# Kernel optimization log

Hardware: AMD Instinct MI355X
Metric: run time of the kernel (lower is better)

## Reference

```python
import jax, jax.numpy as jnp
import numpy as np

N, E, G = 40000, 640000, 64
D_IN, D_EMB, D_HID, D_OUT = 128, 128, 128, 36


def setup_inputs() -> dict:
    key = jax.random.key(0)
    ks = jax.random.split(key, 12)
    x = jax.random.normal(ks[0], (N, D_IN), dtype=jnp.float32)
    edge_weight = jax.random.uniform(ks[1], (E,), dtype=jnp.float32)
    rho = jax.random.uniform(ks[2], (G,), dtype=jnp.float32)
    edge_index = jax.random.randint(ks[3], (2, E), 0, N, dtype=jnp.int32)
    batch = jnp.sort(jax.random.randint(ks[4], (N,), 0, G, dtype=jnp.int32))
    def lin(k, fi, fo):
        s = 1.0 / np.sqrt(fi)
        return jax.random.normal(k, (fi, fo), dtype=jnp.float32) * s
    conv_w = lin(ks[5], D_IN, D_EMB)
    conv_b = jnp.zeros((D_EMB,), jnp.float32)
    w1 = lin(ks[6], 2 * D_EMB + 1, D_HID); b1 = jnp.zeros((D_HID,), jnp.float32)
    w2 = lin(ks[7], D_HID, D_HID);        b2 = jnp.zeros((D_HID,), jnp.float32)
    w3 = lin(ks[8], D_HID, D_OUT);        b3 = jnp.zeros((D_OUT,), jnp.float32)
    return dict(x=x, edge_weight=edge_weight, rho=rho, conv_w=conv_w, conv_b=conv_b,
                w1=w1, b1=b1, w2=w2, b2=b2, w3=w3, b3=b3,
                edge_index=edge_index, batch=batch)


def _gcn_conv(h, edge_index, ew, W, b):
    # PyG GCNConv: add self-loops (weight 1), symmetric deg^-1/2 normalization,
    # linear transform, gather-scale-scatter aggregation, bias.
    n = h.shape[0]
    loop = jnp.arange(n, dtype=edge_index.dtype)
    src = jnp.concatenate([edge_index[0], loop])
    dst = jnp.concatenate([edge_index[1], loop])
    w_all = jnp.concatenate([ew, jnp.ones((n,), ew.dtype)])
    deg = jax.ops.segment_sum(w_all, dst, num_segments=n)
    dinv = jnp.where(deg > 0, jax.lax.rsqrt(deg), 0.0)
    norm = dinv[src] * w_all * dinv[dst]          # [E+N]
    hW = h @ W                                    # [N, D_EMB]
    msg = hW[src] * norm[:, None]                 # [E+N, D_EMB]
    return jax.ops.segment_sum(msg, dst, num_segments=n) + b


def reference(x, edge_weight, rho, conv_w, conv_b, w1, b1, w2, b2, w3, b3,
              edge_index, batch):
    h = jax.nn.relu(_gcn_conv(x, edge_index, edge_weight, conv_w, conv_b))
    g = G
    cnt = jax.ops.segment_sum(jnp.ones((h.shape[0],), h.dtype), batch, num_segments=g)
    hmax = jax.ops.segment_max(h, batch, num_segments=g)
    hmax = jnp.where(cnt[:, None] > 0, hmax, 0.0)
    hsum = jax.ops.segment_sum(h, batch, num_segments=g)
    hmean = hsum / jnp.maximum(cnt, 1.0)[:, None]
    hg = jnp.concatenate([hmax, hmean, rho[:, None]], axis=1)  # [G, 2*D_EMB+1]
    z = jax.nn.relu(hg @ w1 + b1)
    z = jax.nn.relu(z @ w2 + b2)
    return z @ w3 + b3
```

## Files before the change

### kernel.cpp

```cpp
#include <hip/hip_runtime.h>
#include <hip/hip_fp16.h>

static __device__ __forceinline__ float relu_f(float v) { return v > 0.f ? v : 0.f; }

typedef _Float16 half8 __attribute__((ext_vector_type(8)));
typedef float floatx4 __attribute__((ext_vector_type(4)));

#define ELL 96

static __device__ __forceinline__ float entry_w(unsigned int pk) {
  return __half2float(__ushort_as_half((unsigned short)(pk >> 16)));
}


__global__ void init_kernel(unsigned long long* __restrict__ cnt, int n,
                            float* __restrict__ gmax, float* __restrict__ gsum,
                            float* __restrict__ gcnt, int gch, int g,
                            const float* __restrict__ W, _Float16* __restrict__ wt) {
  int i = blockIdx.x * blockDim.x + threadIdx.x;
  if (i < n) cnt[i] = 0ull;
  if (i < gch) { gmax[i] = 0.f; gsum[i] = 0.f; }
  if (i < g) gcnt[i] = 0.f;
  if (i < 128 * 128) {
    int k = i >> 7, nn = i & 127;
    wt[nn * 128 + k] = (_Float16)W[i];
  }
}


__global__ void count_fill_kernel(const int* __restrict__ src, const int* __restrict__ dst,
                                  const float* __restrict__ ew,
                                  unsigned long long* __restrict__ cnt,
                                  unsigned int* __restrict__ epack, int E) {
  int e = blockIdx.x * blockDim.x + threadIdx.x;
  if (e >= E) return;
  int d = dst[e];
  float w = ew[e];
  unsigned long long pk = (1ull << 32) | (unsigned long long)__float2uint_rn(w * 16777216.f);
  unsigned long long old = atomicAdd(&cnt[d], pk);
  unsigned int r = (unsigned int)(old >> 32);
  if (r < ELL) {
    unsigned short w16 = __half_as_ushort(__float2half_rn(w));
    epack[(size_t)d * ELL + r] = (unsigned int)src[e] | ((unsigned int)w16 << 16);
  }
}


__global__ void premul_cast_kernel(const float4* __restrict__ x4,
                                   const unsigned long long* __restrict__ cnt,
                                   half8* __restrict__ xh8, int n) {
  int j = blockIdx.x * blockDim.x + threadIdx.x;
  if (j >= n * 16) return;
  int node = j >> 4;
  unsigned long long cv = cnt[node];
  float deg = 1.f + (float)(unsigned int)cv * (1.f / 16777216.f);
  float dinv = rsqrtf(deg);
  float4 a = x4[2 * j], b = x4[2 * j + 1];
  half8 o;
  o[0] = (_Float16)(a.x * dinv); o[1] = (_Float16)(a.y * dinv);
  o[2] = (_Float16)(a.z * dinv); o[3] = (_Float16)(a.w * dinv);
  o[4] = (_Float16)(b.x * dinv); o[5] = (_Float16)(b.y * dinv);
  o[6] = (_Float16)(b.z * dinv); o[7] = (_Float16)(b.w * dinv);
  xh8[j] = o;
}


__global__ __launch_bounds__(256) void agg_gemm_pool_kernel(const half8* __restrict__ xh8,
    const unsigned long long* __restrict__ cnt,
    const unsigned int* __restrict__ epack, const _Float16* __restrict__ wt,
    const float* __restrict__ bias, const int* __restrict__ batch,
    float* __restrict__ gmax, float* __restrict__ gsum, float* __restrict__ gcnt, int n) {
  __shared__ float sH[64 * 129];
  _Float16* sAgg = (_Float16*)sH;
  __shared__ int sBatch[64];
  int tid = threadIdx.x;
  int w = tid >> 6, lane = tid & 63;
  int grp = lane >> 4, sub = lane & 15;
  int quad = lane >> 4, c15 = lane & 15;
  int row0 = blockIdx.x * 64;
  int nb = n - row0; if (nb > 64) nb = 64;

  #pragma unroll
  for (int it = 0; it < 4; ++it) {
    int rloc = w * 16 + it * 4 + grp;
    int node = row0 + rloc;
    if (node >= n) node = n - 1;
    unsigned long long cv = cnt[node];
    int deg = (int)(unsigned int)(cv >> 32);
    if (deg > ELL) deg = ELL;
    float dn = rsqrtf(1.f + (float)(unsigned int)cv * (1.f / 16777216.f));
    half8 xv = xh8[(size_t)node * 16 + sub];
    float acc[8];
    #pragma unroll
    for (int c = 0; c < 8; ++c) acc[c] = dn * (float)xv[c];
    size_t base = (size_t)node * ELL;
    int dlen = (deg + 7) & ~7;
    for (int j = 0; j < dlen; j += 8) {
      uint4 pa = *(const uint4*)&epack[base + j];
      uint4 pb = *(const uint4*)&epack[base + j + 4];
      unsigned int pk[8] = {pa.x, pa.y, pa.z, pa.w, pb.x, pb.y, pb.z, pb.w};
      half8 hx[8];
      #pragma unroll
      for (int u = 0; u < 8; ++u) {
        int sidx = (j + u < deg) ? (int)(pk[u] & 0xFFFFu) : node;
        hx[u] = xh8[(size_t)sidx * 16 + sub];
      }
      #pragma unroll
      for (int u = 0; u < 8; ++u) {
        float wgt = (j + u < deg) ? entry_w(pk[u]) * dn : 0.f;
        #pragma unroll
        for (int c = 0; c < 8; ++c) acc[c] += wgt * (float)hx[u][c];
      }
    }
    half8 outv;
    #pragma unroll
    for (int c = 0; c < 8; ++c) outv[c] = (_Float16)acc[c];
    *(half8*)&sAgg[rloc * 136 + sub * 8] = outv;
  }
  __syncthreads();

  half8 af[4];
  #pragma unroll
  for (int ks = 0; ks < 4; ++ks)
    af[ks] = *(const half8*)&sAgg[(w * 16 + c15) * 136 + ks * 32 + quad * 8];
  if (tid < nb) sBatch[tid] = batch[row0 + tid];
  __syncthreads();

  float bb[8];
  #pragma unroll
  for (int j = 0; j < 8; ++j) bb[j] = bias[j * 16 + c15];

  floatx4 acc[8] = {};
  #pragma unroll
  for (int ks = 0; ks < 4; ++ks) {
    #pragma unroll
    for (int j = 0; j < 8; ++j) {
      const half8* bptr =
          (const half8*)(wt + (size_t)(j * 16 + c15) * 128 + ks * 32 + quad * 8);
      acc[j] = __builtin_amdgcn_mfma_f32_16x16x32_f16(af[ks], *bptr, acc[j], 0, 0, 0);
    }
  }

  #pragma unroll
  for (int j = 0; j < 8; ++j) {
    int col = j * 16 + c15;
    #pragma unroll
    for (int r = 0; r < 4; ++r) {
      int row = w * 16 + quad * 4 + r;
      if (row < nb) sH[row * 129 + col] = relu_f(acc[j][r] + bb[j]);
    }
  }
  __syncthreads();

  if (tid < 128) {
    int c = tid;
    int cur = sBatch[0];
    float mx = 0.f, sm = 0.f;
    int cnt_ = 0;
    for (int r = 0; r < nb; ++r) {
      int g = sBatch[r];
      if (g != cur) {
        atomicMax((int*)&gmax[cur * 128 + c], __float_as_int(mx));
        atomicAdd(&gsum[cur * 128 + c], sm);
        if (c == 0) atomicAdd(&gcnt[cur], (float)cnt_);
        mx = 0.f; sm = 0.f; cnt_ = 0; cur = g;
      }
      float v = sH[r * 129 + c];
      mx = fmaxf(mx, v);
      sm += v;
      ++cnt_;
    }
    atomicMax((int*)&gmax[cur * 128 + c], __float_as_int(mx));
    atomicAdd(&gsum[cur * 128 + c], sm);
    if (c == 0) atomicAdd(&gcnt[cur], (float)cnt_);
  }
}


__global__ __launch_bounds__(128) void mlp_kernel(const float* __restrict__ gmax,
    const float* __restrict__ gsum, const float* __restrict__ gcnt,
    const float* __restrict__ rho,
    const float* __restrict__ w1, const float* __restrict__ b1,
    const float* __restrict__ w2, const float* __restrict__ b2,
    const float* __restrict__ w3, const float* __restrict__ b3,
    float* __restrict__ out) {
  __shared__ float s_in[257];
  __shared__ float s_z1[128];
  __shared__ float s_z2[128];
  int g = blockIdx.x, t = threadIdx.x;
  float inv_cnt = 1.f / fmaxf(gcnt[g], 1.f);
  s_in[t] = gmax[g * 128 + t];
  s_in[128 + t] = gsum[g * 128 + t] * inv_cnt;
  if (t == 0) s_in[256] = rho[g];
  __syncthreads();
  float s = b1[t];
  for (int k = 0; k < 257; ++k) s += s_in[k] * w1[k * 128 + t];
  s_z1[t] = relu_f(s);
  __syncthreads();
  s = b2[t];
  for (int k = 0; k < 128; ++k) s += s_z1[k] * w2[k * 128 + t];
  s_z2[t] = relu_f(s);
  __syncthreads();
  if (t < 36) {
    s = b3[t];
    for (int k = 0; k < 128; ++k) s += s_z2[k] * w3[k * 36 + t];
    out[g * 36 + t] = s;
  }
}


extern "C" void kernel_launch(void* const* d_in, const int* in_sizes, int n_in,
                              void* d_out, int out_size, void* d_ws, size_t ws_size,
                              hipStream_t stream) {
  const float* x      = (const float*)d_in[0];
  const float* ew     = (const float*)d_in[1];
  const float* rho    = (const float*)d_in[2];
  const float* conv_w = (const float*)d_in[3];
  const float* conv_b = (const float*)d_in[4];
  const float* w1 = (const float*)d_in[5];
  const float* b1 = (const float*)d_in[6];
  const float* w2 = (const float*)d_in[7];
  const float* b2 = (const float*)d_in[8];
  const float* w3 = (const float*)d_in[9];
  const float* b3 = (const float*)d_in[10];
  const int* eidx  = (const int*)d_in[11];
  const int* batch = (const int*)d_in[12];

  const int N = in_sizes[0] / 128;
  const int E = in_sizes[1];
  const int G = in_sizes[2];
  const int* srcp = eidx;
  const int* dstp = eidx + E;

  char* p = (char*)d_ws;
  auto carve = [&](size_t bytes) { char* r = p; p += (bytes + 255) & ~(size_t)255; return (void*)r; };
  unsigned long long* cnt  = (unsigned long long*)carve((size_t)N * 8);
  unsigned int*       epack = (unsigned int*)     carve((size_t)N * ELL * 4);
  half8*              xh    = (half8*)            carve((size_t)N * 128 * 2);
  _Float16*           wt    = (_Float16*)         carve((size_t)128 * 128 * 2);
  float*              gmax  = (float*)            carve((size_t)G * 128 * 4);
  float*              gsum  = (float*)            carve((size_t)G * 128 * 4);
  float*              gcnt  = (float*)            carve((size_t)G * 4);

  int m = N;
  if (G * 128 > m) m = G * 128;
  if (128 * 128 > m) m = 128 * 128;

  init_kernel<<<(m + 255) / 256, 256, 0, stream>>>(cnt, N, gmax, gsum, gcnt,
                                                   G * 128, G, conv_w, wt);
  count_fill_kernel<<<(E + 255) / 256, 256, 0, stream>>>(srcp, dstp, ew, cnt, epack, E);
  premul_cast_kernel<<<(N * 16 + 255) / 256, 256, 0, stream>>>((const float4*)x, cnt, xh, N);
  agg_gemm_pool_kernel<<<(N + 63) / 64, 256, 0, stream>>>(xh, cnt, epack, wt, conv_b,
                                                          batch, gmax, gsum, gcnt, N);
  mlp_kernel<<<G, 128, 0, stream>>>(gmax, gsum, gcnt, rho, w1, b1, w2, b2, w3, b3,
                                    (float*)d_out);
}
```

Baseline: 190.9 us.

## Replace init kernel with memset, vectorize edge fill, prefetch ELL rows, split MLP

Removes the separate init kernel by grouping the zeroed buffers contiguously and clearing them with one hipMemsetAsync, and folds the weight transpose into the edge-fill kernel. The fill kernel now loads four edges per thread with vector loads. The aggregation loop software-prefetches the next ELL chunk of packed edges. The MLP runs with 256 threads, splitting each dot product across two halves and reducing through shared memory. Together these aim to cut launch count, memory-load latency and serial MLP depth, at the cost of extra registers and shared-memory syncs.

New measurement: 210.2 us. +10.1%, slower.

```diff
diff --git a/kernel.cpp b/kernel.cpp
--- a/kernel.cpp
+++ b/kernel.cpp
@@ -13,35 +13,48 @@
 }
 
 
-__global__ void init_kernel(unsigned long long* __restrict__ cnt, int n,
-                            float* __restrict__ gmax, float* __restrict__ gsum,
-                            float* __restrict__ gcnt, int gch, int g,
-                            const float* __restrict__ W, _Float16* __restrict__ wt) {
+__global__ __launch_bounds__(256) void count_fill_kernel(
+    const int* __restrict__ src, const int* __restrict__ dst,
+    const float* __restrict__ ew, unsigned long long* __restrict__ cnt,
+    unsigned int* __restrict__ epack, int E,
+    const float* __restrict__ W, _Float16* __restrict__ wt) {
   int i = blockIdx.x * blockDim.x + threadIdx.x;
-  if (i < n) cnt[i] = 0ull;
-  if (i < gch) { gmax[i] = 0.f; gsum[i] = 0.f; }
-  if (i < g) gcnt[i] = 0.f;
   if (i < 128 * 128) {
     int k = i >> 7, nn = i & 127;
     wt[nn * 128 + k] = (_Float16)W[i];
   }
-}
-
-
-__global__ void count_fill_kernel(const int* __restrict__ src, const int* __restrict__ dst,
-                                  const float* __restrict__ ew,
-                                  unsigned long long* __restrict__ cnt,
-                                  unsigned int* __restrict__ epack, int E) {
-  int e = blockIdx.x * blockDim.x + threadIdx.x;
-  if (e >= E) return;
-  int d = dst[e];
-  float w = ew[e];
-  unsigned long long pk = (1ull << 32) | (unsigned long long)__float2uint_rn(w * 16777216.f);
-  unsigned long long old = atomicAdd(&cnt[d], pk);
-  unsigned int r = (unsigned int)(old >> 32);
-  if (r < ELL) {
-    unsigned short w16 = __half_as_ushort(__float2half_rn(w));
-    epack[(size_t)d * ELL + r] = (unsigned int)src[e] | ((unsigned int)w16 << 16);
+  int e0 = i * 4;
+  if (e0 >= E) return;
+  if (e0 + 3 < E) {
+    int4   s4 = *(const int4*)(src + e0);
+    int4   d4 = *(const int4*)(dst + e0);
+    float4 w4 = *(const float4*)(ew + e0);
+    int   ss[4] = {s4.x, s4.y, s4.z, s4.w};
+    int   dd[4] = {d4.x, d4.y, d4.z, d4.w};
+    float ww[4] = {w4.x, w4.y, w4.z, w4.w};
+    #pragma unroll
+    for (int u = 0; u < 4; ++u) {
+      unsigned long long pk = (1ull << 32) |
+          (unsigned long long)__float2uint_rn(ww[u] * 16777216.f);
+      unsigned long long old = atomicAdd(&cnt[dd[u]], pk);
+      unsigned int r = (unsigned int)(old >> 32);
+      if (r < ELL) {
+        unsigned short w16 = __half_as_ushort(__float2half_rn(ww[u]));
+        epack[(size_t)dd[u] * ELL + r] = (unsigned int)ss[u] | ((unsigned int)w16 << 16);
+      }
+    }
+  } else {
+    for (int e = e0; e < E; ++e) {
+      float w = ew[e];
+      unsigned long long pk = (1ull << 32) |
+          (unsigned long long)__float2uint_rn(w * 16777216.f);
+      unsigned long long old = atomicAdd(&cnt[dst[e]], pk);
+      unsigned int r = (unsigned int)(old >> 32);
+      if (r < ELL) {
+        unsigned short w16 = __half_as_ushort(__float2half_rn(w));
+        epack[(size_t)dst[e] * ELL + r] = (unsigned int)src[e] | ((unsigned int)w16 << 16);
+      }
+    }
   }
 }
 
@@ -95,9 +108,15 @@
     for (int c = 0; c < 8; ++c) acc[c] = dn * (float)xv[c];
     size_t base = (size_t)node * ELL;
     int dlen = (deg + 7) & ~7;
+    uint4 pa, pb;
+    if (dlen > 0) {
+      pa = *(const uint4*)&epack[base];
+      pb = *(const uint4*)&epack[base + 4];
+    }
     for (int j = 0; j < dlen; j += 8) {
-      uint4 pa = *(const uint4*)&epack[base + j];
-      uint4 pb = *(const uint4*)&epack[base + j + 4];
+      size_t nxt = (j + 8 < dlen) ? base + j + 8 : base;
+      uint4 na = *(const uint4*)&epack[nxt];
+      uint4 nb2 = *(const uint4*)&epack[nxt + 4];
       unsigned int pk[8] = {pa.x, pa.y, pa.z, pa.w, pb.x, pb.y, pb.z, pb.w};
       half8 hx[8];
       #pragma unroll
@@ -111,6 +130,7 @@
         #pragma unroll
         for (int c = 0; c < 8; ++c) acc[c] += wgt * (float)hx[u][c];
       }
+      pa = na; pb = nb2;
     }
     half8 outv;
     #pragma unroll
@@ -177,7 +197,7 @@
 }
 
 
-__global__ __launch_bounds__(128) void mlp_kernel(const float* __restrict__ gmax,
+__global__ __launch_bounds__(256) void mlp_kernel(const float* __restrict__ gmax,
     const float* __restrict__ gsum, const float* __restrict__ gcnt,
     const float* __restrict__ rho,
     const float* __restrict__ w1, const float* __restrict__ b1,
@@ -185,27 +205,46 @@
     const float* __restrict__ w3, const float* __restrict__ b3,
     float* __restrict__ out) {
   __shared__ float s_in[257];
+  __shared__ float s_part[256];
   __shared__ float s_z1[128];
   __shared__ float s_z2[128];
   int g = blockIdx.x, t = threadIdx.x;
+  int col = t & 127, seg = t >> 7;
   float inv_cnt = 1.f / fmaxf(gcnt[g], 1.f);
-  s_in[t] = gmax[g * 128 + t];
-  s_in[128 + t] = gsum[g * 128 + t] * inv_cnt;
-  if (t == 0) s_in[256] = rho[g];
-  __syncthreads();
-  float s = b1[t];
-  for (int k = 0; k < 257; ++k) s += s_in[k] * w1[k * 128 + t];
-  s_z1[t] = relu_f(s);
-  __syncthreads();
-  s = b2[t];
-  for (int k = 0; k < 128; ++k) s += s_z1[k] * w2[k * 128 + t];
-  s_z2[t] = relu_f(s);
-  __syncthreads();
-  if (t < 36) {
-    s = b3[t];
-    for (int k = 0; k < 128; ++k) s += s_z2[k] * w3[k * 36 + t];
-    out[g * 36 + t] = s;
-  }
+  if (t < 128) s_in[t] = gmax[g * 128 + t];
+  else         s_in[t] = gsum[g * 128 + (t - 128)] * inv_cnt;
+  if (t == 0)  s_in[256] = rho[g];
+  __syncthreads();
+
+  float s = seg ? 0.f : b1[col];
+  {
+    int k0 = seg ? 128 : 0, k1 = seg ? 257 : 128;
+    for (int k = k0; k < k1; ++k) s += s_in[k] * w1[k * 128 + col];
+  }
+  s_part[t] = s;
+  __syncthreads();
+  if (t < 128) s_z1[t] = relu_f(s_part[t] + s_part[t + 128]);
+  __syncthreads();
+
+  s = seg ? 0.f : b2[col];
+  {
+    int k0 = seg * 64;
+    for (int k = k0; k < k0 + 64; ++k) s += s_z1[k] * w2[k * 128 + col];
+  }
+  s_part[t] = s;
+  __syncthreads();
+  if (t < 128) s_z2[t] = relu_f(s_part[t] + s_part[t + 128]);
+  __syncthreads();
+
+  if (t < 72) {
+    int oc = t % 36, sg = t / 36;
+    s = sg ? 0.f : b3[oc];
+    int k0 = sg * 64;
+    for (int k = k0; k < k0 + 64; ++k) s += s_z2[k] * w3[k * 36 + oc];
+    s_part[t] = s;
+  }
+  __syncthreads();
+  if (t < 36) out[g * 36 + t] = s_part[t] + s_part[t + 36];
 }
 
 
@@ -234,24 +273,25 @@
 
   char* p = (char*)d_ws;
   auto carve = [&](size_t bytes) { char* r = p; p += (bytes + 255) & ~(size_t)255; return (void*)r; };
+  char* zbase = p;
   unsigned long long* cnt  = (unsigned long long*)carve((size_t)N * 8);
-  unsigned int*       epack = (unsigned int*)     carve((size_t)N * ELL * 4);
-  half8*              xh    = (half8*)            carve((size_t)N * 128 * 2);
-  _Float16*           wt    = (_Float16*)         carve((size_t)128 * 128 * 2);
-  float*              gmax  = (float*)            carve((size_t)G * 128 * 4);
-  float*              gsum  = (float*)            carve((size_t)G * 128 * 4);
-  float*              gcnt  = (float*)            carve((size_t)G * 4);
-
-  int m = N;
-  if (G * 128 > m) m = G * 128;
-  if (128 * 128 > m) m = 128 * 128;
-
-  init_kernel<<<(m + 255) / 256, 256, 0, stream>>>(cnt, N, gmax, gsum, gcnt,
-                                                   G * 128, G, conv_w, wt);
-  count_fill_kernel<<<(E + 255) / 256, 256, 0, stream>>>(srcp, dstp, ew, cnt, epack, E);
+  float*              gmax = (float*)             carve((size_t)G * 128 * 4);
+  float*              gsum = (float*)             carve((size_t)G * 128 * 4);
+  float*              gcnt = (float*)             carve((size_t)G * 4);
+  size_t zbytes = (size_t)(p - zbase);
+  unsigned int* epack = (unsigned int*)carve((size_t)N * ELL * 4);
+  half8*        xh    = (half8*)       carve((size_t)N * 128 * 2);
+  _Float16*     wt    = (_Float16*)    carve((size_t)128 * 128 * 2);
+
+  hipMemsetAsync(zbase, 0, zbytes, stream);
+
+  int nthr_cf = (E + 3) / 4;
+  if (nthr_cf < 128 * 128) nthr_cf = 128 * 128;
+  count_fill_kernel<<<(nthr_cf + 255) / 256, 256, 0, stream>>>(srcp, dstp, ew, cnt,
+                                                               epack, E, conv_w, wt);
   premul_cast_kernel<<<(N * 16 + 255) / 256, 256, 0, stream>>>((const float4*)x, cnt, xh, N);
   agg_gemm_pool_kernel<<<(N + 63) / 64, 256, 0, stream>>>(xh, cnt, epack, wt, conv_b,
                                                           batch, gmax, gsum, gcnt, N);
-  mlp_kernel<<<G, 128, 0, stream>>>(gmax, gsum, gcnt, rho, w1, b1, w2, b2, w3, b3,
+  mlp_kernel<<<G, 256, 0, stream>>>(gmax, gsum, gcnt, rho, w1, b1, w2, b2, w3, b3,
                                     (float*)d_out);
 }
```
